# Performance work log

Measured on AMD Instinct MI355X. Metric: run time of the kernel, lower is better.

## Reference

```python
import jax, jax.numpy as jnp
import numpy as np


def _maxpool3(x):
    # 3x3 max pool, stride 1, SAME padding (NHWC), matches tf.keras MaxPooling2D
    return jax.lax.reduce_window(
        x, -jnp.inf, jax.lax.max,
        window_dimensions=(1, 3, 3, 1),
        window_strides=(1, 1, 1, 1),
        padding='SAME')


def setup_inputs() -> dict:
    key = jax.random.key(0)
    scores = jax.random.uniform(key, (16, 1024, 1024, 1), dtype=jnp.float32)
    return {"scores": scores}


def reference(scores):
    zeros = jnp.zeros_like(scores)
    max_mask = scores == _maxpool3(scores)
    for _ in range(2):
        supp_mask = _maxpool3(max_mask.astype(scores.dtype)) > 0
        supp_scores = jnp.where(supp_mask, zeros, scores)
        new_max_mask = supp_scores == _maxpool3(supp_scores)
        max_mask = max_mask | (new_max_mask & ~supp_mask)
    return jnp.where(max_mask, scores, zeros)
```

## Files before the change

### kernel.cpp

```cpp
#include <hip/hip_runtime.h>

#define IMG 1024
#define RH  32
#define NBANDS (IMG / RH)
#define NSTRIP 5
#define NEG_INF (-__builtin_inff())
#define PMASK 0x01010101u

__device__ __forceinline__ unsigned dpp_shr1_u(unsigned x) {
    return (unsigned)__builtin_amdgcn_update_dpp(0, (int)x, 0x138, 0xf, 0xf, true);
}
__device__ __forceinline__ unsigned dpp_shl1_u(unsigned x) {
    return (unsigned)__builtin_amdgcn_update_dpp(0, (int)x, 0x130, 0xf, 0xf, true);
}
__device__ __forceinline__ float dpp_shr1_f(float x) { return __uint_as_float(dpp_shr1_u(__float_as_uint(x))); }
__device__ __forceinline__ float dpp_shl1_f(float x) { return __uint_as_float(dpp_shl1_u(__float_as_uint(x))); }

__device__ __forceinline__ float max3f(float a, float b, float c) { return fmaxf(fmaxf(a, b), c); }

__device__ __forceinline__ float4 vmax3(float4 a, float4 b, float4 c) {
    return make_float4(max3f(a.x,b.x,c.x), max3f(a.y,b.y,c.y),
                       max3f(a.z,b.z,c.z), max3f(a.w,b.w,c.w));
}

__device__ __forceinline__ float4 hmax3(float4 f, bool l0, bool l63) {
    float sl = dpp_shr1_f(f.w);
    float sr = dpp_shl1_f(f.x);
    float L = l0  ? NEG_INF : sl;
    float R = l63 ? NEG_INF : sr;
    return make_float4(max3f(L,   f.x, f.y), max3f(f.x, f.y, f.z),
                       max3f(f.y, f.z, f.w), max3f(f.z, f.w, R));
}

__device__ __forceinline__ unsigned hor3(unsigned p) {
    unsigned sl = dpp_shr1_u(p);
    unsigned sr = dpp_shl1_u(p);
    return ((p | (p << 8) | (p >> 8)) & PMASK) | ((sl >> 24) & 1u) | ((sr & 1u) << 24);
}

__device__ __forceinline__ unsigned cmp_plane(float4 a, float4 m) {
    return (a.x == m.x ? 0x1u : 0u) | (a.y == m.y ? 0x100u : 0u) |
           (a.z == m.z ? 0x10000u : 0u) | (a.w == m.w ? 0x1000000u : 0u);
}

__device__ __forceinline__ float4 supsel(unsigned plane, float4 v) {
    return make_float4(((plane >>  0) & 1u) ? 0.f : v.x,
                       ((plane >>  8) & 1u) ? 0.f : v.y,
                       ((plane >> 16) & 1u) ? 0.f : v.z,
                       ((plane >> 24) & 1u) ? 0.f : v.w);
}

__device__ __forceinline__ float bsel(unsigned bits, int sh, float v) {
    return ((bits >> sh) & 1u) ? v : 0.f;
}

__device__ __forceinline__ unsigned vmask(int r, int lmax) {
    return ((unsigned)r < (unsigned)lmax) ? PMASK : 0u;
}

#define STEP(K) do {                                                                    \
    const int s_ = sb + (K);                                                            \
                                                          \
    HV[(K)+2] = hmax3(H[9+(K)], l0, l63);                                               \
                                                                    \
    float4 vm0 = vmax3(HV[(K)+2], HV[(K)+1], HV[(K)]);                                  \
    unsigned m0n = cmp_plane(H[8+(K)], vm0) & vmask(s_ - 2, lmax);                      \
    m0h = ((m0h << 1) & ~PMASK) | m0n;                                                  \
                                                                   \
    unsigned hm0n = hor3((m0h >> 1) & PMASK);                                           \
    hm0h = ((hm0h << 1) & ~PMASK) | hm0n;                                               \
                                                                 \
    unsigned s1n = (hm0h | (hm0h >> 1) | (hm0h >> 2)) & PMASK;                          \
    s1h = ((s1h << 1) & ~PMASK) | s1n;                                                  \
                      \
    SS1[(K)+2] = supsel(s1n & vmask(s_ - 4, lmax), H[6+(K)]);                           \
                                                             \
    H1[(K)+2] = hmax3(SS1[(K)+1], l0, l63);                                             \
                                                                 \
    float4 vm1 = vmax3(H1[(K)+2], H1[(K)+1], H1[(K)]);                                  \
    unsigned s1l2 = (s1h >> 2) & PMASK;                                                 \
    unsigned nm1 = cmp_plane(SS1[(K)], vm1) & vmask(s_ - 6, lmax);                      \
    unsigned mk1n = ((m0h >> 4) & PMASK) | (nm1 & ~s1l2);                               \
    mk1h = ((mk1h << 1) & ~PMASK) | mk1n;                                               \
                                                                  \
    unsigned hm1n = hor3((mk1h >> 1) & PMASK);                                          \
    hm1h = ((hm1h << 1) & ~PMASK) | hm1n;                                               \
                                                                \
    unsigned s2n = (hm1h | (hm1h >> 1) | (hm1h >> 2)) & PMASK;                          \
    s2h = ((s2h << 1) & ~PMASK) | s2n;                                                  \
                                                 \
    SS2[(K)+2] = supsel(s2n & vmask(s_ - 8, lmax), H[2+(K)]);                           \
                                                            \
    H2[(K)+2] = hmax3(SS2[(K)+1], l0, l63);                                             \
                                                      \
    float4 vm2 = vmax3(H2[(K)+2], H2[(K)+1], H2[(K)]);                                  \
    unsigned s2l2 = (s2h >> 2) & PMASK;                                                 \
    unsigned nm2 = cmp_plane(SS2[(K)], vm2) & vmask(s_ - 10, lmax);                     \
    unsigned mk2 = ((mk1h >> 4) & PMASK) | (nm2 & ~s2l2);                               \
    const int srow = s_ - 10;                                                           \
    if (srow >= y0 && srow < yend && ok_lane) {                                         \
        float4 vv = H[(K)];                                                             \
        outp4[(size_t)srow * (IMG/4) + cb4 + lane] = make_float4(                       \
            bsel(mk2, 0, vv.x), bsel(mk2, 8, vv.y),                                     \
            bsel(mk2, 16, vv.z), bsel(mk2, 24, vv.w));                                  \
    }                                                                                   \
} while (0)

__global__ __launch_bounds__(256, 2)
void nms_sweep(const float* __restrict__ in, float* __restrict__ out)
{
    const int tid  = threadIdx.x;
    const int lane = tid & 63;
    const int w    = tid >> 6;
    const bool l0  = (lane == 0);
    const bool l63 = (lane == 63);

    const int wid   = (int)blockIdx.x * 4 + w;
    const int strip = wid / NBANDS;
    const int band  = wid - strip * NBANDS;
    const int y0    = band * RH;
    const int yend  = y0 + RH;
    const int cb    = strip * 240;
    const int cb4   = cb >> 2;
    const size_t base = (size_t)blockIdx.y * ((size_t)IMG * IMG);
    const int lmax  = (yend + 5 < IMG) ? yend + 5 : IMG;

    const float4* inp4  = (const float4*)(in + base);
    float4*       outp4 = (float4*)(out + base);

    const int lc = cb + 4 * lane;
    const bool col_ok = lc < IMG;
    const int lo_off = (strip == 0) ? 0 : 8;
    const int hi_off = (IMG - cb < 248) ? (IMG - cb) : 248;
    const bool ok_lane = (4 * lane >= lo_off) && (4 * lane + 4 <= hi_off);

    const float4 ninf4 = make_float4(NEG_INF, NEG_INF, NEG_INF, NEG_INF);
    float4 H[14], Hn[4], HV[6], SS1[6], H1[6], SS2[6], H2[6];
#pragma unroll
    for (int i = 0; i < 14; ++i) H[i] = ninf4;
#pragma unroll
    for (int i = 0; i < 6; ++i) { HV[i] = ninf4; H1[i] = ninf4; H2[i] = ninf4; SS1[i] = ninf4; SS2[i] = ninf4; }
    unsigned m0h = 0, hm0h = 0, s1h = 0, mk1h = 0, hm1h = 0, s2h = 0;

    int sb = y0 - 5;

#pragma unroll
    for (int k = 0; k < 4; ++k) {
        const int r = sb + k;
        H[10 + k] = (col_ok && (unsigned)r < (unsigned)lmax) ? inp4[(size_t)r * (IMG/4) + cb4 + lane] : ninf4;
    }

#pragma unroll 1
    for (int it = 0; it < (RH + 15 + 3) / 4; ++it) {
#pragma unroll
        for (int k = 0; k < 4; ++k) {
            const int r = sb + 4 + k;
            Hn[k] = (col_ok && (unsigned)r < (unsigned)lmax) ? inp4[(size_t)r * (IMG/4) + cb4 + lane] : ninf4;
        }

        STEP(0);
        STEP(1);
        STEP(2);
        STEP(3);

#pragma unroll
        for (int i = 0; i < 10; ++i) H[i] = H[i + 4];
        H[10] = Hn[0]; H[11] = Hn[1]; H[12] = Hn[2]; H[13] = Hn[3];
        HV[0] = HV[4];   HV[1] = HV[5];
        SS1[0] = SS1[4]; SS1[1] = SS1[5];
        H1[0] = H1[4];   H1[1] = H1[5];
        SS2[0] = SS2[4]; SS2[1] = SS2[5];
        H2[0] = H2[4];   H2[1] = H2[5];
        sb += 4;
    }
}

extern "C" void kernel_launch(void* const* d_in, const int* in_sizes, int n_in,
                              void* d_out, int out_size, void* d_ws, size_t ws_size,
                              hipStream_t stream) {
    const float* in = (const float*)d_in[0];
    float* out = (float*)d_out;
    const int batch = in_sizes[0] / (IMG * IMG);
    dim3 grid((NSTRIP * NBANDS) / 4, batch, 1);
    nms_sweep<<<grid, dim3(256, 1, 1), 0, stream>>>(in, out);
}
```

Measured before the change: 52.92 us.

## Switch to one column per lane with wave-ballot bitmasks for NMS masks

Restructures the sweep so each lane handles a single column instead of a float4, with strips narrowed to 48 output columns plus an 8-column halo on each side. Per-stage masks become 64-bit wave ballots, so horizontal dilation is plain shifts of scalar bitmasks and per-row mask history is kept in small u64 arrays instead of packed byte planes. The aim is to cut vector ALU work for mask bookkeeping by moving it to scalar registers and ops. In exchange, the halo overhead per strip grows, so more redundant loads and max computation are done, and the loads shrink to 4 bytes per lane.

Result: slower. 70.58 us (+33.4%).

```diff
diff --git a/kernel.cpp b/kernel.cpp
--- a/kernel.cpp
+++ b/kernel.cpp
@@ -1,109 +1,80 @@
 #include <hip/hip_runtime.h>
+
+typedef unsigned long long u64;
 
 #define IMG 1024
 #define RH  32
 #define NBANDS (IMG / RH)
-#define NSTRIP 5
+#define OUTW 48
+#define NSTRIP 22
 #define NEG_INF (-__builtin_inff())
-#define PMASK 0x01010101u
 
-__device__ __forceinline__ unsigned dpp_shr1_u(unsigned x) {
-    return (unsigned)__builtin_amdgcn_update_dpp(0, (int)x, 0x138, 0xf, 0xf, true);
+__device__ __forceinline__ float dpp_shr1_f(float x) {
+    return __uint_as_float((unsigned)__builtin_amdgcn_update_dpp(0, (int)__float_as_uint(x), 0x138, 0xf, 0xf, true));
 }
-__device__ __forceinline__ unsigned dpp_shl1_u(unsigned x) {
-    return (unsigned)__builtin_amdgcn_update_dpp(0, (int)x, 0x130, 0xf, 0xf, true);
+__device__ __forceinline__ float dpp_shl1_f(float x) {
+    return __uint_as_float((unsigned)__builtin_amdgcn_update_dpp(0, (int)__float_as_uint(x), 0x130, 0xf, 0xf, true));
 }
-__device__ __forceinline__ float dpp_shr1_f(float x) { return __uint_as_float(dpp_shr1_u(__float_as_uint(x))); }
-__device__ __forceinline__ float dpp_shl1_f(float x) { return __uint_as_float(dpp_shl1_u(__float_as_uint(x))); }
 
 __device__ __forceinline__ float max3f(float a, float b, float c) { return fmaxf(fmaxf(a, b), c); }
 
-__device__ __forceinline__ float4 vmax3(float4 a, float4 b, float4 c) {
-    return make_float4(max3f(a.x,b.x,c.x), max3f(a.y,b.y,c.y),
-                       max3f(a.z,b.z,c.z), max3f(a.w,b.w,c.w));
+__device__ __forceinline__ bool lane_bit(u64 m, int lane) {
+#if __has_builtin(__builtin_amdgcn_inverse_ballot_w64)
+    (void)lane;
+    return __builtin_amdgcn_inverse_ballot_w64(m);
+#else
+    return ((m >> (unsigned)lane) & 1ull) != 0ull;
+#endif
 }
 
-__device__ __forceinline__ float4 hmax3(float4 f, bool l0, bool l63) {
-    float sl = dpp_shr1_f(f.w);
-    float sr = dpp_shl1_f(f.x);
-    float L = l0  ? NEG_INF : sl;
-    float R = l63 ? NEG_INF : sr;
-    return make_float4(max3f(L,   f.x, f.y), max3f(f.x, f.y, f.z),
-                       max3f(f.y, f.z, f.w), max3f(f.z, f.w, R));
+__device__ __forceinline__ float cnd_zero(float v, u64 m, int lane) {
+    return lane_bit(m, lane) ? 0.f : v;
+}
+__device__ __forceinline__ float cnd_keep(float v, u64 m, int lane) {
+    return lane_bit(m, lane) ? v : 0.f;
 }
 
-__device__ __forceinline__ unsigned hor3(unsigned p) {
-    unsigned sl = dpp_shr1_u(p);
-    unsigned sr = dpp_shl1_u(p);
-    return ((p | (p << 8) | (p >> 8)) & PMASK) | ((sl >> 24) & 1u) | ((sr & 1u) << 24);
-}
+__device__ __forceinline__ u64 hor3s(u64 m) { return m | (m << 1) | (m >> 1); }
 
-__device__ __forceinline__ unsigned cmp_plane(float4 a, float4 m) {
-    return (a.x == m.x ? 0x1u : 0u) | (a.y == m.y ? 0x100u : 0u) |
-           (a.z == m.z ? 0x10000u : 0u) | (a.w == m.w ? 0x1000000u : 0u);
-}
+#define RV(r) (((unsigned)(r) < (unsigned)lmax) ? ~0ull : 0ull)
 
-__device__ __forceinline__ float4 supsel(unsigned plane, float4 v) {
-    return make_float4(((plane >>  0) & 1u) ? 0.f : v.x,
-                       ((plane >>  8) & 1u) ? 0.f : v.y,
-                       ((plane >> 16) & 1u) ? 0.f : v.z,
-                       ((plane >> 24) & 1u) ? 0.f : v.w);
-}
-
-__device__ __forceinline__ float bsel(unsigned bits, int sh, float v) {
-    return ((bits >> sh) & 1u) ? v : 0.f;
-}
-
-__device__ __forceinline__ unsigned vmask(int r, int lmax) {
-    return ((unsigned)r < (unsigned)lmax) ? PMASK : 0u;
-}
-
-#define STEP(K) do {                                                                    \
-    const int s_ = sb + (K);                                                            \
-                                                          \
-    HV[(K)+2] = hmax3(H[9+(K)], l0, l63);                                               \
-                                                                    \
-    float4 vm0 = vmax3(HV[(K)+2], HV[(K)+1], HV[(K)]);                                  \
-    unsigned m0n = cmp_plane(H[8+(K)], vm0) & vmask(s_ - 2, lmax);                      \
-    m0h = ((m0h << 1) & ~PMASK) | m0n;                                                  \
-                                                                   \
-    unsigned hm0n = hor3((m0h >> 1) & PMASK);                                           \
-    hm0h = ((hm0h << 1) & ~PMASK) | hm0n;                                               \
-                                                                 \
-    unsigned s1n = (hm0h | (hm0h >> 1) | (hm0h >> 2)) & PMASK;                          \
-    s1h = ((s1h << 1) & ~PMASK) | s1n;                                                  \
-                      \
-    SS1[(K)+2] = supsel(s1n & vmask(s_ - 4, lmax), H[6+(K)]);                           \
-                                                             \
-    H1[(K)+2] = hmax3(SS1[(K)+1], l0, l63);                                             \
-                                                                 \
-    float4 vm1 = vmax3(H1[(K)+2], H1[(K)+1], H1[(K)]);                                  \
-    unsigned s1l2 = (s1h >> 2) & PMASK;                                                 \
-    unsigned nm1 = cmp_plane(SS1[(K)], vm1) & vmask(s_ - 6, lmax);                      \
-    unsigned mk1n = ((m0h >> 4) & PMASK) | (nm1 & ~s1l2);                               \
-    mk1h = ((mk1h << 1) & ~PMASK) | mk1n;                                               \
+#define STEP(K) do {                                                                     \
+    const int s_ = sb + (K);                                                             \
+    const u64 rv2 = RV(s_-2), rv4 = RV(s_-4), rv6 = RV(s_-6), rv8 = RV(s_-8), rv10 = RV(s_-10); \
+                                                               \
+    HV[(K)+2] = max3f(dpp_shr1_f(H[9+(K)]), H[9+(K)], dpp_shl1_f(H[9+(K)]));             \
+                                                                         \
+    float vm0 = max3f(HV[(K)+2], HV[(K)+1], HV[(K)]);                                    \
+    M0[(K)+4] = __ballot(H[8+(K)] == vm0) & rv2 & cvm;                                   \
+                                                                        \
+    HM0[(K)+2] = hor3s(M0[(K)+3]);                                                       \
+                                                                      \
+    S1A[(K)+2] = HM0[(K)+2] | HM0[(K)+1] | HM0[(K)];                                     \
+                                                                        \
+    SS1[(K)+2] = cnd_zero(H[6+(K)], S1A[(K)+2] & rv4, lane);                             \
                                                                   \
-    unsigned hm1n = hor3((mk1h >> 1) & PMASK);                                          \
-    hm1h = ((hm1h << 1) & ~PMASK) | hm1n;                                               \
-                                                                \
-    unsigned s2n = (hm1h | (hm1h >> 1) | (hm1h >> 2)) & PMASK;                          \
-    s2h = ((s2h << 1) & ~PMASK) | s2n;                                                  \
-                                                 \
-    SS2[(K)+2] = supsel(s2n & vmask(s_ - 8, lmax), H[2+(K)]);                           \
+    H1[(K)+2] = max3f(dpp_shr1_f(SS1[(K)+1]), SS1[(K)+1], dpp_shl1_f(SS1[(K)+1]));       \
+                                                                      \
+    float vm1 = max3f(H1[(K)+2], H1[(K)+1], H1[(K)]);                                    \
+    u64 nm1 = __ballot(SS1[(K)] == vm1) & rv6 & cvm;                                     \
+    MK1[(K)+4] = M0[(K)] | (nm1 & ~S1A[(K)]);                                            \
+                                                                        \
+    HM1[(K)+2] = hor3s(MK1[(K)+3]);                                                      \
+                                                                      \
+    S2A[(K)+2] = HM1[(K)+2] | HM1[(K)+1] | HM1[(K)];                                     \
+                                                                        \
+    SS2[(K)+2] = cnd_zero(H[2+(K)], S2A[(K)+2] & rv8, lane);                             \
+                                                                  \
+    H2[(K)+2] = max3f(dpp_shr1_f(SS2[(K)+1]), SS2[(K)+1], dpp_shl1_f(SS2[(K)+1]));       \
                                                             \
-    H2[(K)+2] = hmax3(SS2[(K)+1], l0, l63);                                             \
-                                                      \
-    float4 vm2 = vmax3(H2[(K)+2], H2[(K)+1], H2[(K)]);                                  \
-    unsigned s2l2 = (s2h >> 2) & PMASK;                                                 \
-    unsigned nm2 = cmp_plane(SS2[(K)], vm2) & vmask(s_ - 10, lmax);                     \
-    unsigned mk2 = ((mk1h >> 4) & PMASK) | (nm2 & ~s2l2);                               \
-    const int srow = s_ - 10;                                                           \
-    if (srow >= y0 && srow < yend && ok_lane) {                                         \
-        float4 vv = H[(K)];                                                             \
-        outp4[(size_t)srow * (IMG/4) + cb4 + lane] = make_float4(                       \
-            bsel(mk2, 0, vv.x), bsel(mk2, 8, vv.y),                                     \
-            bsel(mk2, 16, vv.z), bsel(mk2, 24, vv.w));                                  \
-    }                                                                                   \
+    float vm2 = max3f(H2[(K)+2], H2[(K)+1], H2[(K)]);                                    \
+    u64 nm2 = __ballot(SS2[(K)] == vm2) & rv10 & cvm;                                    \
+    u64 mk2 = MK1[(K)] | (nm2 & ~S2A[(K)]);                                              \
+    const int srow = s_ - 10;                                                            \
+    if (srow >= y0 && srow < yend) {                                 \
+        float ov = cnd_keep(H[(K)], mk2, lane);                                          \
+        if (out_ok) opl[(size_t)srow * IMG] = ov;                                        \
+    }                                                                                    \
 } while (0)
 
 __global__ __launch_bounds__(256, 2)
@@ -112,42 +83,40 @@
     const int tid  = threadIdx.x;
     const int lane = tid & 63;
     const int w    = tid >> 6;
-    const bool l0  = (lane == 0);
-    const bool l63 = (lane == 63);
 
     const int wid   = (int)blockIdx.x * 4 + w;
     const int strip = wid / NBANDS;
     const int band  = wid - strip * NBANDS;
     const int y0    = band * RH;
     const int yend  = y0 + RH;
-    const int cb    = strip * 240;
-    const int cb4   = cb >> 2;
     const size_t base = (size_t)blockIdx.y * ((size_t)IMG * IMG);
     const int lmax  = (yend + 5 < IMG) ? yend + 5 : IMG;
 
-    const float4* inp4  = (const float4*)(in + base);
-    float4*       outp4 = (float4*)(out + base);
+    const int col     = strip * OUTW - 8 + lane;
+    const bool col_ok = (unsigned)col < (unsigned)IMG;
+    const bool out_ok = (lane >= 8) && (lane < 8 + OUTW) && (col < IMG);
+    const u64  cvm    = __ballot(col_ok);
 
-    const int lc = cb + 4 * lane;
-    const bool col_ok = lc < IMG;
-    const int lo_off = (strip == 0) ? 0 : 8;
-    const int hi_off = (IMG - cb < 248) ? (IMG - cb) : 248;
-    const bool ok_lane = (4 * lane >= lo_off) && (4 * lane + 4 <= hi_off);
+    const float* ipl = in  + base + col;
+    float*       opl = out + base + col;
 
-    const float4 ninf4 = make_float4(NEG_INF, NEG_INF, NEG_INF, NEG_INF);
-    float4 H[14], Hn[4], HV[6], SS1[6], H1[6], SS2[6], H2[6];
+    float H[14], Hn[4], HV[6], SS1[6], H1[6], SS2[6], H2[6];
 #pragma unroll
-    for (int i = 0; i < 14; ++i) H[i] = ninf4;
+    for (int i = 0; i < 14; ++i) H[i] = NEG_INF;
 #pragma unroll
-    for (int i = 0; i < 6; ++i) { HV[i] = ninf4; H1[i] = ninf4; H2[i] = ninf4; SS1[i] = ninf4; SS2[i] = ninf4; }
-    unsigned m0h = 0, hm0h = 0, s1h = 0, mk1h = 0, hm1h = 0, s2h = 0;
+    for (int i = 0; i < 6; ++i) { HV[i]=NEG_INF; SS1[i]=NEG_INF; H1[i]=NEG_INF; SS2[i]=NEG_INF; H2[i]=NEG_INF; }
+    u64 M0[8], HM0[6], S1A[6], MK1[8], HM1[6], S2A[6];
+#pragma unroll
+    for (int i = 0; i < 8; ++i) { M0[i] = 0; MK1[i] = 0; }
+#pragma unroll
+    for (int i = 0; i < 6; ++i) { HM0[i] = 0; S1A[i] = 0; HM1[i] = 0; S2A[i] = 0; }
 
     int sb = y0 - 5;
 
 #pragma unroll
     for (int k = 0; k < 4; ++k) {
         const int r = sb + k;
-        H[10 + k] = (col_ok && (unsigned)r < (unsigned)lmax) ? inp4[(size_t)r * (IMG/4) + cb4 + lane] : ninf4;
+        H[10 + k] = (col_ok && (unsigned)r < (unsigned)lmax) ? ipl[(size_t)r * IMG] : NEG_INF;
     }
 
 #pragma unroll 1
@@ -155,7 +124,7 @@
 #pragma unroll
         for (int k = 0; k < 4; ++k) {
             const int r = sb + 4 + k;
-            Hn[k] = (col_ok && (unsigned)r < (unsigned)lmax) ? inp4[(size_t)r * (IMG/4) + cb4 + lane] : ninf4;
+            Hn[k] = (col_ok && (unsigned)r < (unsigned)lmax) ? ipl[(size_t)r * IMG] : NEG_INF;
         }
 
         STEP(0);
@@ -166,11 +135,17 @@
 #pragma unroll
         for (int i = 0; i < 10; ++i) H[i] = H[i + 4];
         H[10] = Hn[0]; H[11] = Hn[1]; H[12] = Hn[2]; H[13] = Hn[3];
-        HV[0] = HV[4];   HV[1] = HV[5];
-        SS1[0] = SS1[4]; SS1[1] = SS1[5];
-        H1[0] = H1[4];   H1[1] = H1[5];
-        SS2[0] = SS2[4]; SS2[1] = SS2[5];
-        H2[0] = H2[4];   H2[1] = H2[5];
+        HV[0]=HV[4];   HV[1]=HV[5];
+        SS1[0]=SS1[4]; SS1[1]=SS1[5];
+        H1[0]=H1[4];   H1[1]=H1[5];
+        SS2[0]=SS2[4]; SS2[1]=SS2[5];
+        H2[0]=H2[4];   H2[1]=H2[5];
+        M0[0]=M0[4];   M0[1]=M0[5];   M0[2]=M0[6];   M0[3]=M0[7];
+        MK1[0]=MK1[4]; MK1[1]=MK1[5]; MK1[2]=MK1[6]; MK1[3]=MK1[7];
+        HM0[0]=HM0[4]; HM0[1]=HM0[5];
+        S1A[0]=S1A[4]; S1A[1]=S1A[5];
+        HM1[0]=HM1[4]; HM1[1]=HM1[5];
+        S2A[0]=S2A[4]; S2A[1]=S2A[5];
         sb += 4;
     }
 }
```
